# Performance work log

Measured on AMD Instinct MI355X. Metric: run time of the kernel, lower is better.

## Reference

```python
import jax, jax.numpy as jnp
import numpy as np

# Mamba2 hyperparameters
D_MODEL = 768
D_STATE = 64
D_CONV = 4
EXPAND = 2
HEADDIM = 64
CHUNK = 64
D_INNER = EXPAND * D_MODEL            # 1536
NHEADS = D_INNER // HEADDIM           # 24
D_IN_PROJ = 2 * D_INNER + 2 * D_STATE + NHEADS  # 3224
CONV_DIM = D_INNER + 2 * D_STATE      # 1664
B_SZ = 8
SEQ = 4096  # multiple of CHUNK -> no padding branch


def setup_inputs() -> dict:
    key = jax.random.key(0)
    ks = jax.random.split(key, 6)
    u = jax.random.normal(ks[0], (B_SZ, SEQ, D_MODEL), jnp.float32)
    # fan-in scaled weights (matches nn.Linear/Conv1d default init scale)
    W_in = jax.random.normal(ks[1], (D_IN_PROJ, D_MODEL), jnp.float32) / np.sqrt(D_MODEL).astype(np.float32)
    conv_w = jax.random.normal(ks[2], (CONV_DIM, 1, D_CONV), jnp.float32) / np.sqrt(D_CONV).astype(np.float32)
    conv_b = jnp.zeros((CONV_DIM,), jnp.float32)
    dt_bias = jax.random.uniform(ks[3], (NHEADS,), jnp.float32, -4.0, 1.0)  # nn.init.uniform_(-4, 1)
    A_log = jnp.full((NHEADS,), -np.log(2.0), jnp.float32)                  # nn.init.constant_(-log 2)
    D_param = jnp.ones((NHEADS,), jnp.float32)
    norm_w = jnp.ones((D_INNER,), jnp.float32)
    W_out = jax.random.normal(ks[4], (D_MODEL, D_INNER), jnp.float32) / np.sqrt(D_INNER).astype(np.float32)
    return dict(u=u, W_in=W_in, conv_w=conv_w, conv_b=conv_b, dt_bias=dt_bias,
                A_log=A_log, D_param=D_param, norm_w=norm_w, W_out=W_out)


def _segsum(x):
    """Stable segment sum: out[..., i, j] = sum_{j < k <= i} x[..., k]; -inf above diagonal."""
    T = x.shape[-1]
    lower_strict = jnp.tril(jnp.ones((T, T), bool), -1)
    xe = jnp.where(lower_strict, x[..., :, None], 0.0)   # broadcast x over last (col) axis
    s = jnp.cumsum(xe, axis=-2)
    lower = jnp.tril(jnp.ones((T, T), bool), 0)
    return jnp.where(lower, s, -jnp.inf)


def _ssd(x, A, B, C, chunk):
    """Chunked SSD. x:(b,L,h,p)  A:(b,L,h)  B,C:(b,L,1,n)."""
    b, L, h, p = x.shape
    c = L // chunk
    n = B.shape[-1]
    x = x.reshape(b, c, chunk, h, p)
    A = A.reshape(b, c, chunk, h).transpose(0, 3, 1, 2)   # b h c l
    B = B.reshape(b, c, chunk, 1, n)
    C = C.reshape(b, c, chunk, 1, n)
    A_cs = jnp.cumsum(A, axis=-1)                          # b h c l
    # intra-chunk (diagonal) term
    Lmat = jnp.exp(_segsum(A))                             # b h c l s
    Y_diag = jnp.einsum('bclhn,bcshn,bhcls,bcshp->bclhp', C, B, Lmat, x)
    # per-chunk states
    decay_states = jnp.exp(A_cs[..., -1:] - A_cs)          # b h c l
    states = jnp.einsum('bclhn,bhcl,bclhp->bchpn', B, decay_states, x)
    states = jnp.concatenate([jnp.zeros_like(states[:, :1]), states], axis=1)  # b (c+1) h p n
    # inter-chunk recurrence
    A_last = jnp.pad(A_cs[..., -1], ((0, 0), (0, 0), (1, 0)))  # b h (c+1)
    decay_chunk = jnp.exp(_segsum(A_last))                     # b h (c+1) (c+1)
    new_states = jnp.einsum('bhzc,bchpn->bzhpn', decay_chunk, states)
    states = new_states[:, :-1]                                # b c h p n
    # off-diagonal (state-to-output) term
    Y_off = jnp.einsum('bclhn,bchpn,bhcl->bclhp', C, states, jnp.exp(A_cs))
    return (Y_diag + Y_off).reshape(b, L, h, p)


def reference(u, W_in, conv_w, conv_b, dt_bias, A_log, D_param, norm_w, W_out):
    b, L, _ = u.shape  # L % CHUNK == 0, so pad branch is a no-op
    zxbcdt = u @ W_in.T                                    # (b, L, D_IN_PROJ)
    z = zxbcdt[..., :D_INNER]
    xBC = zxbcdt[..., D_INNER:D_INNER + CONV_DIM]
    dt = jax.nn.softplus(zxbcdt[..., D_INNER + CONV_DIM:] + dt_bias)  # (b, L, h)
    # causal depthwise conv1d (torch pads both sides by d_conv-1 then slices [:L] == left pad)
    xBC = jax.lax.conv_general_dilated(
        xBC.transpose(0, 2, 1), conv_w, window_strides=(1,),
        padding=[(D_CONV - 1, 0)], dimension_numbers=('NCH', 'OIH', 'NCH'),
        feature_group_count=CONV_DIM)
    xBC = jax.nn.silu(xBC.transpose(0, 2, 1) + conv_b)     # (b, L, CONV_DIM)
    x = xBC[..., :D_INNER].reshape(b, L, NHEADS, HEADDIM)
    Bm = xBC[..., D_INNER:D_INNER + D_STATE][:, :, None, :]  # (b, L, 1, n)
    Cm = xBC[..., D_INNER + D_STATE:][:, :, None, :]
    A = -jnp.exp(A_log)                                    # (h,)
    Y = _ssd(x * dt[..., None], A * dt, Bm, Cm, CHUNK)
    y = Y + x * D_param[:, None]                           # skip term
    y = y.reshape(b, L, D_INNER)
    # gated RMSNorm: x * silu(z), then rmsnorm * weight
    y = y * jax.nn.silu(z)
    y = y * jax.lax.rsqrt(jnp.mean(y * y, axis=-1, keepdims=True) + 1e-5) * norm_w
    return y @ W_out.T
```

## Files before the change

### kernel.cpp

```cpp
#include <hip/hip_runtime.h>
#include <stdint.h>

typedef unsigned short u16;
typedef __bf16 bf16x8 __attribute__((ext_vector_type(8)));
typedef float f32x4 __attribute__((ext_vector_type(4)));
typedef unsigned short u16x8 __attribute__((ext_vector_type(8)));
typedef unsigned short u16x4 __attribute__((ext_vector_type(4)));
typedef __attribute__((address_space(1))) unsigned int gu32;
typedef __attribute__((address_space(3))) unsigned int lu32;

__device__ __forceinline__ float bf2f(u16 u){ unsigned int v=((unsigned int)u)<<16; float f; __builtin_memcpy(&f,&v,4); return f; }
__device__ __forceinline__ u16 f2bf(float f){ unsigned int v; __builtin_memcpy(&v,&f,4); v += 0x7fffu + ((v>>16)&1u); return (u16)(v>>16); }
__device__ __forceinline__ int swz(int r,int c){ return (r<<6) + (c ^ ((r&7)<<3)); }
__device__ __forceinline__ void glds16(const void* g, void* l){
  __builtin_amdgcn_global_load_lds((gu32*)g, (lu32*)l, 16, 0, 0);
}

__global__ __launch_bounds__(256) void k_cast(const float* __restrict__ in, u16* __restrict__ out, int n4){
  int i = blockIdx.x*256 + threadIdx.x;
  if (i >= n4) return;
  const f32x4 v = *(const f32x4*)(in + (size_t)i*4);
  u16x4 o; o.x=f2bf(v.x); o.y=f2bf(v.y); o.z=f2bf(v.z); o.w=f2bf(v.w);
  *(u16x4*)(out + (size_t)i*4) = o;
}

__global__ __launch_bounds__(256) void k_cast_pad(const float* __restrict__ in, u16* __restrict__ out){
  int i = blockIdx.x*256 + threadIdx.x;
  int e0 = i*4;
  int row = e0 / 768;
  int col = e0 - row*768;
  u16x4 o;
  if (row < 3224){
    const f32x4 v = *(const f32x4*)(in + (size_t)row*768 + col);
    o.x=f2bf(v.x); o.y=f2bf(v.y); o.z=f2bf(v.z); o.w=f2bf(v.w);
  } else { o.x=0; o.y=0; o.z=0; o.w=0; }
  *(u16x4*)(out + e0) = o;
}

template<int K, int EPI>
__global__ __launch_bounds__(256,2) void k_gemm(
    const u16* __restrict__ A, const u16* __restrict__ Bw,
    u16* __restrict__ o_z, u16* __restrict__ o_xbc, float* __restrict__ o_dt,
    const float* __restrict__ dt_bias, float* __restrict__ o_f32)
{
  __shared__ __align__(16) u16 Alds[8192];
  __shared__ __align__(16) u16 Blds[8192];
  const int tid = threadIdx.x;
  const int wave = tid>>6, lane = tid&63;
  const int m0 = blockIdx.x<<7, n0 = blockIdx.y<<7;
  const int wr = (wave>>1)<<6, wc = (wave&1)<<6;
  const int srow = tid>>3, sc0 = (tid&7)<<3;
  const int lo16 = lane&15, hi = lane>>4;
  f32x4 acc[4][4] = {};
  for (int k0 = 0; k0 < K; k0 += 64){
    #pragma unroll
    for (int i = 0; i < 4; ++i){
      const int row = (i<<5) + srow;
      const int scol = sc0 ^ ((row&7)<<3);
      glds16(A  + (size_t)(m0+row)*K + k0 + scol, &Alds[(i<<11) + (wave<<9)]);
      glds16(Bw + (size_t)(n0+row)*K + k0 + scol, &Blds[(i<<11) + (wave<<9)]);
    }
    __syncthreads();
    #pragma unroll
    for (int kk = 0; kk < 2; ++kk){
      const int kb = (kk<<5) + (hi<<3);
      bf16x8 af[4], bfv[4];
      #pragma unroll
      for (int m = 0; m < 4; ++m){
        const int r = wr + (m<<4) + lo16;
        af[m] = *(const bf16x8*)&Alds[(r<<6) + (kb ^ ((r&7)<<3))];
      }
      #pragma unroll
      for (int n = 0; n < 4; ++n){
        const int r = wc + (n<<4) + lo16;
        bfv[n] = *(const bf16x8*)&Blds[(r<<6) + (kb ^ ((r&7)<<3))];
      }
      #pragma unroll
      for (int m = 0; m < 4; ++m)
      #pragma unroll
      for (int n = 0; n < 4; ++n)
        acc[m][n] = __builtin_amdgcn_mfma_f32_16x16x32_bf16(af[m], bfv[n], acc[m][n], 0,0,0);
    }
    __syncthreads();
  }
  #pragma unroll
  for (int m = 0; m < 4; ++m)
  #pragma unroll
  for (int n = 0; n < 4; ++n)
  #pragma unroll
  for (int i = 0; i < 4; ++i){
    const int gr = m0 + wr + (m<<4) + (hi<<2) + i;
    const int gc = n0 + wc + (n<<4) + lo16;
    const float v = acc[m][n][i];
    if constexpr (EPI == 0){
      if (gc < 1536)      o_z[(size_t)gr*1536 + gc] = f2bf(v);
      else if (gc < 3200) o_xbc[(size_t)gr*1664 + (gc-1536)] = f2bf(v);
      else if (gc < 3224){
        const float t = v + dt_bias[gc-3200];
        o_dt[(size_t)gr*24 + (gc-3200)] = (t > 20.f) ? t : log1pf(__expf(t));
      }
    } else {
      o_f32[(size_t)gr*768 + gc] = v;
    }
  }
}

__global__ __launch_bounds__(256) void k_conv(
    const u16* __restrict__ xbc, const float* __restrict__ cw, const float* __restrict__ cb,
    u16* __restrict__ xo, u16* __restrict__ Bo, u16* __restrict__ Co)
{
  const int idx = blockIdx.x*256 + threadIdx.x;
  if (idx >= 4096*208) return;
  const int g  = idx % 208;
  const int pt = idx / 208;
  const int ch0 = g << 3;
  const int m0 = pt << 3;
  const int l0 = m0 & 4095;
  float wgt[8][4], bias[8];
  #pragma unroll
  for (int j = 0; j < 8; ++j){
    const f32x4 wv = *(const f32x4*)(cw + (size_t)(ch0+j)*4);
    wgt[j][0]=wv.x; wgt[j][1]=wv.y; wgt[j][2]=wv.z; wgt[j][3]=wv.w;
    bias[j] = cb[ch0+j];
  }
  float acc[8][8];
  #pragma unroll
  for (int p = 0; p < 8; ++p)
  #pragma unroll
  for (int j = 0; j < 8; ++j) acc[p][j] = bias[j];
  #pragma unroll
  for (int r = -3; r < 8; ++r){
    const int ls = l0 + r;
    if (ls < 0) continue;
    const u16x8 v = *(const u16x8*)(xbc + (size_t)(m0+r)*1664 + ch0);
    float xf[8];
    #pragma unroll
    for (int j = 0; j < 8; ++j) xf[j] = bf2f(v[j]);
    #pragma unroll
    for (int t = 0; t < 4; ++t){
      const int p = r + 3 - t;
      if (p < 0 || p > 7) continue;
      #pragma unroll
      for (int j = 0; j < 8; ++j) acc[p][j] += xf[j] * wgt[j][t];
    }
  }
  #pragma unroll
  for (int p = 0; p < 8; ++p){
    u16x8 o;
    #pragma unroll
    for (int j = 0; j < 8; ++j){ const float s = acc[p][j]; o[j] = f2bf(s / (1.f + __expf(-s))); }
    const size_t m = m0 + p;
    if (ch0 < 1536)      *(u16x8*)(xo + m*1536 + ch0)      = o;
    else if (ch0 < 1600) *(u16x8*)(Bo + m*64 + (ch0-1536)) = o;
    else                 *(u16x8*)(Co + m*64 + (ch0-1600)) = o;
  }
}

__global__ __launch_bounds__(256,1) void k_ssd(
    const u16* __restrict__ xc, const u16* __restrict__ Bg, const u16* __restrict__ Cg,
    const float* __restrict__ dtg, const float* __restrict__ A_log,
    const float* __restrict__ Dp, u16* __restrict__ yo)
{
  __shared__ __align__(16) u16 Bn[4096], Bdt[4096], Cn[4096], Cd[4096], xdtT[4096], xls[4096], Ml[4096], Sbf[4096];
  __shared__ float Sst[4096];
  __shared__ float df[64], Acs[64];
  const int tid = threadIdx.x, wave = tid>>6, lane = tid&63;
  const int lo16 = lane&15, hi = lane>>4;
  const int b = blockIdx.x / 24, h = blockIdx.x % 24;
  const float Ah = -__expf(A_log[h]);
  const float Dh = Dp[h];
  for (int i = tid; i < 4096; i += 256){ Sst[i]=0.f; Sbf[i]=0; }
  const int lrow = tid>>2, c16 = (tid&3)<<4;
  const size_t bx  = (size_t)b*4096*1536 + (size_t)h*64;
  const size_t bbc = (size_t)b*4096*64;
  const size_t bdt = (size_t)b*4096*24 + h;

  for (int c = 0; c < 64; ++c){
    const int l0 = c<<6;
    if (tid < 64) df[tid] = dtg[bdt + (size_t)(l0+tid)*24];
    __syncthreads();
    if (wave == 0){
      float s = Ah * df[lane];
      #pragma unroll
      for (int off = 1; off < 64; off <<= 1){
        const float t = __shfl_up(s, off);
        if (lane >= off) s += t;
      }
      Acs[lane] = s;
    }
    __syncthreads();
    const float Alast = Acs[63];
    {
      const float dtl = df[lrow];
      const float dec = __expf(Alast - Acs[lrow]);
      const float el  = __expf(Acs[lrow]);
      const u16* gx  = xc + bx  + (size_t)(l0+lrow)*1536 + c16;
      const u16* gb  = Bg + bbc + (size_t)(l0+lrow)*64 + c16;
      const u16* gcp = Cg + bbc + (size_t)(l0+lrow)*64 + c16;
      const u16x8 x0 = *(const u16x8*)gx;      const u16x8 x1 = *(const u16x8*)(gx+8);
      const u16x8 b0 = *(const u16x8*)gb;      const u16x8 b1 = *(const u16x8*)(gb+8);
      const u16x8 c0 = *(const u16x8*)gcp;     const u16x8 c1 = *(const u16x8*)(gcp+8);
      #pragma unroll
      for (int j = 0; j < 8; ++j){
        const int p = c16 + j, q = c16 + 8 + j;
        xls[swz(lrow,p)]  = x0[j];                         xls[swz(lrow,q)]  = x1[j];
        xdtT[swz(p,lrow)] = f2bf(bf2f(x0[j]) * dtl);       xdtT[swz(q,lrow)] = f2bf(bf2f(x1[j]) * dtl);
        Bn[swz(lrow,p)]   = b0[j];                         Bn[swz(lrow,q)]   = b1[j];
        Bdt[swz(p,lrow)]  = f2bf(bf2f(b0[j]) * dec);       Bdt[swz(q,lrow)]  = f2bf(bf2f(b1[j]) * dec);
        Cn[swz(lrow,p)]   = c0[j];                         Cn[swz(lrow,q)]   = c1[j];
        Cd[swz(lrow,p)]   = f2bf(bf2f(c0[j]) * el);        Cd[swz(lrow,q)]   = f2bf(bf2f(c1[j]) * el);
      }
    }
    __syncthreads();
    f32x4 accG[4] = {};
    #pragma unroll
    for (int kk = 0; kk < 2; ++kk){
      const int kb = (kk<<5) + (hi<<3);
      const int rA = (wave<<4) + lo16;
      const bf16x8 a = *(const bf16x8*)&Cn[(rA<<6) + (kb ^ ((rA&7)<<3))];
      #pragma unroll
      for (int t = 0; t < 4; ++t){
        const int rb = (t<<4) + lo16;
        const bf16x8 bb = *(const bf16x8*)&Bn[(rb<<6) + (kb ^ ((rb&7)<<3))];
        accG[t] = __builtin_amdgcn_mfma_f32_16x16x32_bf16(a, bb, accG[t], 0,0,0);
      }
    }
    #pragma unroll
    for (int t = 0; t < 4; ++t)
    #pragma unroll
    for (int i = 0; i < 4; ++i){
      const int r = (wave<<4) + (hi<<2) + i;
      const int s = (t<<4) + lo16;
      const float v = (s <= r) ? accG[t][i] * __expf(Acs[r] - Acs[s]) : 0.f;
      Ml[swz(r,s)] = f2bf(v);
    }
    f32x4 accY[4] = {}, accS[4] = {};
    #pragma unroll
    for (int kk = 0; kk < 2; ++kk){
      const int kb = (kk<<5) + (hi<<3);
      const int rA = (wave<<4) + lo16;
      const int oA = (rA<<6) + (kb ^ ((rA&7)<<3));
      const bf16x8 aM = *(const bf16x8*)&Ml[oA];
      const bf16x8 aC = *(const bf16x8*)&Cd[oA];
      const bf16x8 aX = *(const bf16x8*)&xdtT[oA];
      #pragma unroll
      for (int t = 0; t < 4; ++t){
        const int rb = (t<<4) + lo16;
        const int o = (rb<<6) + (kb ^ ((rb&7)<<3));
        const bf16x8 bX = *(const bf16x8*)&xdtT[o];
        const bf16x8 bS = *(const bf16x8*)&Sbf[o];
        const bf16x8 bB = *(const bf16x8*)&Bdt[o];
        accY[t] = __builtin_amdgcn_mfma_f32_16x16x32_bf16(aM, bX, accY[t], 0,0,0);
        accY[t] = __builtin_amdgcn_mfma_f32_16x16x32_bf16(aC, bS, accY[t], 0,0,0);
        accS[t] = __builtin_amdgcn_mfma_f32_16x16x32_bf16(aX, bB, accS[t], 0,0,0);
      }
    }
    __syncthreads();
    const float lam = __expf(Alast);
    #pragma unroll
    for (int t = 0; t < 4; ++t)
    #pragma unroll
    for (int i = 0; i < 4; ++i){
      const int p = (wave<<4) + (hi<<2) + i;
      const int n = (t<<4) + lo16;
      const float s = Sst[(p<<6)+n] * lam + accS[t][i];
      Sst[(p<<6)+n] = s;
      Sbf[swz(p,n)] = f2bf(s);
    }
    #pragma unroll
    for (int t = 0; t < 4; ++t)
    #pragma unroll
    for (int i = 0; i < 4; ++i){
      const int r = (wave<<4) + (hi<<2) + i;
      const int p = (t<<4) + lo16;
      const float y = accY[t][i] + bf2f(xls[swz(r,p)]) * Dh;
      yo[bx + (size_t)(l0+r)*1536 + p] = f2bf(y);
    }
  }
}

__global__ __launch_bounds__(192) void k_gnorm(
    const u16* __restrict__ y, const u16* __restrict__ z,
    const float* __restrict__ nw, u16* __restrict__ out)
{
  __shared__ float red[3];
  const int m = blockIdx.x, t = threadIdx.x;
  const size_t base = (size_t)m*1536 + t*8;
  const u16x8 yv = *(const u16x8*)(y + base);
  const u16x8 zv = *(const u16x8*)(z + base);
  float vals[8]; float ss = 0.f;
  #pragma unroll
  for (int j = 0; j < 8; ++j){
    const float zf = bf2f(zv[j]);
    const float v = bf2f(yv[j]) * zf / (1.f + __expf(-zf));
    vals[j] = v; ss += v*v;
  }
  #pragma unroll
  for (int off = 32; off > 0; off >>= 1) ss += __shfl_down(ss, off);
  if ((t & 63) == 0) red[t>>6] = ss;
  __syncthreads();
  const float sc = rsqrtf((red[0]+red[1]+red[2]) * (1.f/1536.f) + 1e-5f);
  u16x8 o;
  #pragma unroll
  for (int j = 0; j < 8; ++j) o[j] = f2bf(vals[j] * sc * nw[t*8+j]);
  *(u16x8*)(out + base) = o;
}

extern "C" void kernel_launch(void* const* d_in, const int* in_sizes, int n_in,
                              void* d_out, int out_size, void* d_ws, size_t ws_size,
                              hipStream_t stream)
{
  const float* u       = (const float*)d_in[0];
  const float* W_in    = (const float*)d_in[1];
  const float* conv_w  = (const float*)d_in[2];
  const float* conv_b  = (const float*)d_in[3];
  const float* dt_bias = (const float*)d_in[4];
  const float* A_log   = (const float*)d_in[5];
  const float* D_param = (const float*)d_in[6];
  const float* norm_w  = (const float*)d_in[7];
  const float* W_out   = (const float*)d_in[8];
  (void)in_sizes; (void)n_in; (void)out_size;
  if (ws_size < (size_t)379715584) return;

  char* w = (char*)d_ws;
  size_t off = 0;
  auto alloc = [&](size_t bytes)->void*{ void* p = w + off; off += (bytes + 255) & ~(size_t)255; return p; };
  u16* ubf    = (u16*)alloc(50331648);
  u16* winbf  = (u16*)alloc(5111808);
  u16* woutbf = (u16*)alloc(2359296);
  u16* zbf    = (u16*)alloc(100663296);
  u16* xbcbf  = (u16*)alloc(109051904);
  float* dtbuf= (float*)alloc(3145728);
  u16* xconv  = (u16*)alloc(100663296);
  u16* Bbuf   = (u16*)alloc(4194304);
  u16* Cbuf   = (u16*)alloc(4194304);
  u16* yssd   = xbcbf;
  u16* ynorm  = xconv;

  k_cast<<<24576, 256, 0, stream>>>(u, ubf, 6291456);
  k_cast_pad<<<2496, 256, 0, stream>>>(W_in, winbf);
  k_cast<<<1152, 256, 0, stream>>>(W_out, woutbf, 294912);
  k_gemm<768,0><<<dim3(256,26), 256, 0, stream>>>(ubf, winbf, zbf, xbcbf, dtbuf, dt_bias, nullptr);
  k_conv<<<3328, 256, 0, stream>>>(xbcbf, conv_w, conv_b, xconv, Bbuf, Cbuf);
  k_ssd<<<192, 256, 0, stream>>>(xconv, Bbuf, Cbuf, dtbuf, A_log, D_param, yssd);
  k_gnorm<<<32768, 192, 0, stream>>>(yssd, zbf, norm_w, ynorm);
  k_gemm<1536,1><<<dim3(256,6), 256, 0, stream>>>(ynorm, woutbf, nullptr, nullptr, nullptr, nullptr, (float*)d_out);
}
```

Baseline: 752.4 us.

## Pre-swizzle SSD operands in conv and double-buffer chunk loads in SSD

The conv kernel now writes x*dt transposed and pre-swizzled per chunk, plus B in normal and transposed form and C in normal form, and dt is stored head-major. The SSD kernel then streams these tiles into LDS with async global_load_lds, double-buffered so the next chunk's loads overlap compute. It also folds the D skip term into the diagonal of the intra-chunk matrix (Dh/dt) and applies decay and exp scaling at use time. This removes the per-chunk scalar transpose-and-scale LDS stores and serial global load latency from the 192-block SSD kernel, at the cost of more conv output writes, manual waitcnt tuning, and a possible precision change from dividing by dt in bf16.

```diff
diff --git a/kernel.cpp b/kernel.cpp
--- a/kernel.cpp
+++ b/kernel.cpp
@@ -97,7 +97,7 @@
       else if (gc < 3200) o_xbc[(size_t)gr*1664 + (gc-1536)] = f2bf(v);
       else if (gc < 3224){
         const float t = v + dt_bias[gc-3200];
-        o_dt[(size_t)gr*24 + (gc-3200)] = (t > 20.f) ? t : log1pf(__expf(t));
+        o_dt[(size_t)(gc-3200)*32768 + gr] = (t > 20.f) ? t : log1pf(__expf(t));
       }
     } else {
       o_f32[(size_t)gr*768 + gc] = v;
@@ -107,7 +107,8 @@
 
 __global__ __launch_bounds__(256) void k_conv(
     const u16* __restrict__ xbc, const float* __restrict__ cw, const float* __restrict__ cb,
-    u16* __restrict__ xo, u16* __restrict__ Bo, u16* __restrict__ Co)
+    const float* __restrict__ dtT,
+    u16* __restrict__ xT, u16* __restrict__ Bn, u16* __restrict__ BT, u16* __restrict__ Cn)
 {
   const int idx = blockIdx.x*256 + threadIdx.x;
   if (idx >= 4096*208) return;
@@ -116,18 +117,18 @@
   const int ch0 = g << 3;
   const int m0 = pt << 3;
   const int l0 = m0 & 4095;
-  float wgt[8][4], bias[8];
+  float wgt[8][4], bias8[8];
   #pragma unroll
   for (int j = 0; j < 8; ++j){
     const f32x4 wv = *(const f32x4*)(cw + (size_t)(ch0+j)*4);
     wgt[j][0]=wv.x; wgt[j][1]=wv.y; wgt[j][2]=wv.z; wgt[j][3]=wv.w;
-    bias[j] = cb[ch0+j];
+    bias8[j] = cb[ch0+j];
   }
   float acc[8][8];
   #pragma unroll
   for (int p = 0; p < 8; ++p)
   #pragma unroll
-  for (int j = 0; j < 8; ++j) acc[p][j] = bias[j];
+  for (int j = 0; j < 8; ++j) acc[p][j] = bias8[j];
   #pragma unroll
   for (int r = -3; r < 8; ++r){
     const int ls = l0 + r;
@@ -145,83 +146,128 @@
     }
   }
   #pragma unroll
-  for (int p = 0; p < 8; ++p){
-    u16x8 o;
-    #pragma unroll
-    for (int j = 0; j < 8; ++j){ const float s = acc[p][j]; o[j] = f2bf(s / (1.f + __expf(-s))); }
-    const size_t m = m0 + p;
-    if (ch0 < 1536)      *(u16x8*)(xo + m*1536 + ch0)      = o;
-    else if (ch0 < 1600) *(u16x8*)(Bo + m*64 + (ch0-1536)) = o;
-    else                 *(u16x8*)(Co + m*64 + (ch0-1600)) = o;
+  for (int p = 0; p < 8; ++p)
+  #pragma unroll
+  for (int j = 0; j < 8; ++j){ const float s = acc[p][j]; acc[p][j] = s / (1.f + __expf(-s)); }
+
+  const int b = m0 >> 12;
+  const int cch = l0 >> 6;
+  const int lr0 = l0 & 63;
+  if (ch0 < 1536){
+    const int h = ch0 >> 6, p0 = ch0 & 63;
+    const f32x4 d0 = *(const f32x4*)(dtT + (size_t)h*32768 + m0);
+    const f32x4 d1 = *(const f32x4*)(dtT + (size_t)h*32768 + m0 + 4);
+    const float dtl[8] = {d0.x,d0.y,d0.z,d0.w,d1.x,d1.y,d1.z,d1.w};
+    const size_t rb = (size_t)(b*24+h)*64;
+    #pragma unroll
+    for (int j = 0; j < 8; ++j){
+      const int row = p0 + j;
+      u16x8 o;
+      #pragma unroll
+      for (int p = 0; p < 8; ++p) o[p] = f2bf(acc[p][j] * dtl[p]);
+      *(u16x8*)(xT + (rb + row)*4096 + (size_t)cch*64 + (lr0 ^ ((row&7)<<3))) = o;
+    }
+  } else if (ch0 < 1600){
+    const int n0 = ch0 - 1536;
+    const size_t tb = ((size_t)(b*64 + cch))*4096;
+    #pragma unroll
+    for (int p = 0; p < 8; ++p){
+      const int lr = lr0 + p;
+      u16x8 o;
+      #pragma unroll
+      for (int j = 0; j < 8; ++j) o[j] = f2bf(acc[p][j]);
+      *(u16x8*)(Bn + tb + lr*64 + (n0 ^ ((lr&7)<<3))) = o;
+    }
+    #pragma unroll
+    for (int j = 0; j < 8; ++j){
+      const int row = n0 + j;
+      u16x8 o;
+      #pragma unroll
+      for (int p = 0; p < 8; ++p) o[p] = f2bf(acc[p][j]);
+      *(u16x8*)(BT + tb + row*64 + (lr0 ^ ((row&7)<<3))) = o;
+    }
+  } else {
+    const int n0 = ch0 - 1600;
+    const size_t tb = ((size_t)(b*64 + cch))*4096;
+    #pragma unroll
+    for (int p = 0; p < 8; ++p){
+      const int lr = lr0 + p;
+      u16x8 o;
+      #pragma unroll
+      for (int j = 0; j < 8; ++j) o[j] = f2bf(acc[p][j]);
+      *(u16x8*)(Cn + tb + lr*64 + (n0 ^ ((lr&7)<<3))) = o;
+    }
   }
 }
 
 __global__ __launch_bounds__(256,1) void k_ssd(
-    const u16* __restrict__ xc, const u16* __restrict__ Bg, const u16* __restrict__ Cg,
-    const float* __restrict__ dtg, const float* __restrict__ A_log,
+    const u16* __restrict__ xT, const u16* __restrict__ Bn, const u16* __restrict__ BT,
+    const u16* __restrict__ Cn, const float* __restrict__ dtT, const float* __restrict__ A_log,
     const float* __restrict__ Dp, u16* __restrict__ yo)
 {
-  __shared__ __align__(16) u16 Bn[4096], Bdt[4096], Cn[4096], Cd[4096], xdtT[4096], xls[4096], Ml[4096], Sbf[4096];
+  __shared__ __align__(16) u16 tiles[2][4][4096];
+  __shared__ __align__(16) u16 Ml[4096];
+  __shared__ __align__(16) u16 Sbf[4096];
   __shared__ float Sst[4096];
-  __shared__ float df[64], Acs[64];
+  __shared__ float df[64], Acs[64], decs[64], els[64];
   const int tid = threadIdx.x, wave = tid>>6, lane = tid&63;
   const int lo16 = lane&15, hi = lane>>4;
   const int b = blockIdx.x / 24, h = blockIdx.x % 24;
   const float Ah = -__expf(A_log[h]);
   const float Dh = Dp[h];
   for (int i = tid; i < 4096; i += 256){ Sst[i]=0.f; Sbf[i]=0; }
-  const int lrow = tid>>2, c16 = (tid&3)<<4;
-  const size_t bx  = (size_t)b*4096*1536 + (size_t)h*64;
-  const size_t bbc = (size_t)b*4096*64;
-  const size_t bdt = (size_t)b*4096*24 + h;
+  const size_t xTg  = (size_t)(b*24+h)*64*4096;
+  const size_t bcg  = (size_t)b*64*4096;
+  const size_t dtg0 = (size_t)h*32768 + (size_t)b*4096;
+  const size_t yb   = (size_t)b*4096*1536 + (size_t)h*64;
+
+  auto stage = [&](int buf, int c){
+    u16* dst = &tiles[buf][wave][0];
+    if (wave == 0){
+      const u16* g0 = xT + xTg + (size_t)c*64 + (size_t)(lane>>3)*4096 + (lane&7)*8;
+      #pragma unroll
+      for (int s = 0; s < 8; ++s) glds16(g0 + (size_t)s*32768, dst + s*512);
+    } else {
+      const u16* src = (wave==1 ? Bn : wave==2 ? BT : Cn) + bcg + (size_t)c*4096 + lane*8;
+      #pragma unroll
+      for (int s = 0; s < 8; ++s) glds16(src + s*512, dst + s*512);
+    }
+  };
+
+  float dtc = dtT[dtg0 + lane];
+  stage(0, 0);
 
   for (int c = 0; c < 64; ++c){
-    const int l0 = c<<6;
-    if (tid < 64) df[tid] = dtg[bdt + (size_t)(l0+tid)*24];
-    __syncthreads();
-    if (wave == 0){
-      float s = Ah * df[lane];
-      #pragma unroll
-      for (int off = 1; off < 64; off <<= 1){
-        const float t = __shfl_up(s, off);
-        if (lane >= off) s += t;
-      }
-      Acs[lane] = s;
-    }
-    __syncthreads();
-    const float Alast = Acs[63];
-    {
-      const float dtl = df[lrow];
-      const float dec = __expf(Alast - Acs[lrow]);
-      const float el  = __expf(Acs[lrow]);
-      const u16* gx  = xc + bx  + (size_t)(l0+lrow)*1536 + c16;
-      const u16* gb  = Bg + bbc + (size_t)(l0+lrow)*64 + c16;
-      const u16* gcp = Cg + bbc + (size_t)(l0+lrow)*64 + c16;
-      const u16x8 x0 = *(const u16x8*)gx;      const u16x8 x1 = *(const u16x8*)(gx+8);
-      const u16x8 b0 = *(const u16x8*)gb;      const u16x8 b1 = *(const u16x8*)(gb+8);
-      const u16x8 c0 = *(const u16x8*)gcp;     const u16x8 c1 = *(const u16x8*)(gcp+8);
-      #pragma unroll
-      for (int j = 0; j < 8; ++j){
-        const int p = c16 + j, q = c16 + 8 + j;
-        xls[swz(lrow,p)]  = x0[j];                         xls[swz(lrow,q)]  = x1[j];
-        xdtT[swz(p,lrow)] = f2bf(bf2f(x0[j]) * dtl);       xdtT[swz(q,lrow)] = f2bf(bf2f(x1[j]) * dtl);
-        Bn[swz(lrow,p)]   = b0[j];                         Bn[swz(lrow,q)]   = b1[j];
-        Bdt[swz(p,lrow)]  = f2bf(bf2f(b0[j]) * dec);       Bdt[swz(q,lrow)]  = f2bf(bf2f(b1[j]) * dec);
-        Cn[swz(lrow,p)]   = c0[j];                         Cn[swz(lrow,q)]   = c1[j];
-        Cd[swz(lrow,p)]   = f2bf(bf2f(c0[j]) * el);        Cd[swz(lrow,q)]   = f2bf(bf2f(c1[j]) * el);
-      }
-    }
-    __syncthreads();
+    float s = Ah * dtc;
+    #pragma unroll
+    for (int o = 1; o < 64; o <<= 1){ const float t = __shfl_up(s, o); if (lane >= o) s += t; }
+    const float Alast = __shfl(s, 63);
+    const float lam = __expf(Alast);
+    if (wave == 0){ df[lane] = dtc; Acs[lane] = s; decs[lane] = __expf(Alast - s); els[lane] = __expf(s); }
+    if (c < 63){
+      dtc = dtT[dtg0 + (size_t)(c+1)*64 + lane];
+      stage((c+1)&1, c+1);
+    }
+    if (c == 0)       asm volatile("s_waitcnt vmcnt(0) lgkmcnt(0)" ::: "memory");
+    else if (c == 63) asm volatile("s_waitcnt vmcnt(16) lgkmcnt(0)" ::: "memory");
+    else              asm volatile("s_waitcnt vmcnt(25) lgkmcnt(0)" ::: "memory");
+    __builtin_amdgcn_s_barrier();
+
+    const u16* tx = &tiles[c&1][0][0];
+    const u16* tb = &tiles[c&1][1][0];
+    const u16* tt = &tiles[c&1][2][0];
+    const u16* tc = &tiles[c&1][3][0];
+
     f32x4 accG[4] = {};
     #pragma unroll
     for (int kk = 0; kk < 2; ++kk){
       const int kb = (kk<<5) + (hi<<3);
       const int rA = (wave<<4) + lo16;
-      const bf16x8 a = *(const bf16x8*)&Cn[(rA<<6) + (kb ^ ((rA&7)<<3))];
+      const bf16x8 a = *(const bf16x8*)&tc[(rA<<6) + (kb ^ ((rA&7)<<3))];
       #pragma unroll
       for (int t = 0; t < 4; ++t){
         const int rb = (t<<4) + lo16;
-        const bf16x8 bb = *(const bf16x8*)&Bn[(rb<<6) + (kb ^ ((rb&7)<<3))];
+        const bf16x8 bb = *(const bf16x8*)&tb[(rb<<6) + (kb ^ ((rb&7)<<3))];
         accG[t] = __builtin_amdgcn_mfma_f32_16x16x32_bf16(a, bb, accG[t], 0,0,0);
       }
     }
@@ -230,42 +276,51 @@
     #pragma unroll
     for (int i = 0; i < 4; ++i){
       const int r = (wave<<4) + (hi<<2) + i;
-      const int s = (t<<4) + lo16;
-      const float v = (s <= r) ? accG[t][i] * __expf(Acs[r] - Acs[s]) : 0.f;
-      Ml[swz(r,s)] = f2bf(v);
-    }
-    f32x4 accY[4] = {}, accS[4] = {};
+      const int sc = (t<<4) + lo16;
+      float v = 0.f;
+      if (sc <= r) v = accG[t][i] * __expf(Acs[r] - Acs[sc]);
+      if (sc == r) v += Dh / df[r];
+      Ml[swz(r,sc)] = f2bf(v);
+    }
+    f32x4 aYd[4] = {}, aYo[4] = {}, aS[4] = {};
     #pragma unroll
     for (int kk = 0; kk < 2; ++kk){
       const int kb = (kk<<5) + (hi<<3);
       const int rA = (wave<<4) + lo16;
       const int oA = (rA<<6) + (kb ^ ((rA&7)<<3));
       const bf16x8 aM = *(const bf16x8*)&Ml[oA];
-      const bf16x8 aC = *(const bf16x8*)&Cd[oA];
-      const bf16x8 aX = *(const bf16x8*)&xdtT[oA];
+      const bf16x8 aC = *(const bf16x8*)&tc[oA];
+      const u16x8  aXu = *(const u16x8*)&tx[oA];
+      u16x8 aXsu;
+      #pragma unroll
+      for (int j = 0; j < 8; ++j) aXsu[j] = f2bf(bf2f(aXu[j]) * decs[kb + j]);
+      const bf16x8 aXs = *(const bf16x8*)&aXsu;
       #pragma unroll
       for (int t = 0; t < 4; ++t){
         const int rb = (t<<4) + lo16;
         const int o = (rb<<6) + (kb ^ ((rb&7)<<3));
-        const bf16x8 bX = *(const bf16x8*)&xdtT[o];
+        const bf16x8 bX = *(const bf16x8*)&tx[o];
         const bf16x8 bS = *(const bf16x8*)&Sbf[o];
-        const bf16x8 bB = *(const bf16x8*)&Bdt[o];
-        accY[t] = __builtin_amdgcn_mfma_f32_16x16x32_bf16(aM, bX, accY[t], 0,0,0);
-        accY[t] = __builtin_amdgcn_mfma_f32_16x16x32_bf16(aC, bS, accY[t], 0,0,0);
-        accS[t] = __builtin_amdgcn_mfma_f32_16x16x32_bf16(aX, bB, accS[t], 0,0,0);
+        const bf16x8 bB = *(const bf16x8*)&tt[o];
+        aYd[t] = __builtin_amdgcn_mfma_f32_16x16x32_bf16(aM, bX, aYd[t], 0,0,0);
+        aYo[t] = __builtin_amdgcn_mfma_f32_16x16x32_bf16(aC, bS, aYo[t], 0,0,0);
+        aS[t]  = __builtin_amdgcn_mfma_f32_16x16x32_bf16(aXs, bB, aS[t], 0,0,0);
       }
     }
-    __syncthreads();
-    const float lam = __expf(Alast);
+    float el4[4];
+    #pragma unroll
+    for (int i = 0; i < 4; ++i) el4[i] = els[(wave<<4) + (hi<<2) + i];
+    asm volatile("s_waitcnt lgkmcnt(0)" ::: "memory");
+    __builtin_amdgcn_s_barrier();
     #pragma unroll
     for (int t = 0; t < 4; ++t)
     #pragma unroll
     for (int i = 0; i < 4; ++i){
       const int p = (wave<<4) + (hi<<2) + i;
       const int n = (t<<4) + lo16;
-      const float s = Sst[(p<<6)+n] * lam + accS[t][i];
-      Sst[(p<<6)+n] = s;
-      Sbf[swz(p,n)] = f2bf(s);
+      const float sv = Sst[(p<<6)+n] * lam + aS[t][i];
+      Sst[(p<<6)+n] = sv;
+      Sbf[swz(p,n)] = f2bf(sv);
     }
     #pragma unroll
     for (int t = 0; t < 4; ++t)
@@ -273,8 +328,8 @@
     for (int i = 0; i < 4; ++i){
       const int r = (wave<<4) + (hi<<2) + i;
       const int p = (t<<4) + lo16;
-      const float y = accY[t][i] + bf2f(xls[swz(r,p)]) * Dh;
-      yo[bx + (size_t)(l0+r)*1536 + p] = f2bf(y);
+      const float y = aYd[t][i] + el4[i] * aYo[t][i];
+      yo[yb + (size_t)((c<<6)+r)*1536 + p] = f2bf(y);
     }
   }
 }
@@ -330,19 +385,20 @@
   u16* woutbf = (u16*)alloc(2359296);
   u16* zbf    = (u16*)alloc(100663296);
   u16* xbcbf  = (u16*)alloc(109051904);
-  float* dtbuf= (float*)alloc(3145728);
-  u16* xconv  = (u16*)alloc(100663296);
-  u16* Bbuf   = (u16*)alloc(4194304);
-  u16* Cbuf   = (u16*)alloc(4194304);
+  float* dtT  = (float*)alloc(3145728);
+  u16* xTb    = (u16*)alloc(100663296);
+  u16* Bnb    = (u16*)alloc(4194304);
+  u16* Cnb    = (u16*)alloc(4194304);
+  u16* BTb    = ubf;
   u16* yssd   = xbcbf;
-  u16* ynorm  = xconv;
+  u16* ynorm  = xTb;
 
   k_cast<<<24576, 256, 0, stream>>>(u, ubf, 6291456);
   k_cast_pad<<<2496, 256, 0, stream>>>(W_in, winbf);
   k_cast<<<1152, 256, 0, stream>>>(W_out, woutbf, 294912);
-  k_gemm<768,0><<<dim3(256,26), 256, 0, stream>>>(ubf, winbf, zbf, xbcbf, dtbuf, dt_bias, nullptr);
-  k_conv<<<3328, 256, 0, stream>>>(xbcbf, conv_w, conv_b, xconv, Bbuf, Cbuf);
-  k_ssd<<<192, 256, 0, stream>>>(xconv, Bbuf, Cbuf, dtbuf, A_log, D_param, yssd);
+  k_gemm<768,0><<<dim3(256,26), 256, 0, stream>>>(ubf, winbf, zbf, xbcbf, dtT, dt_bias, nullptr);
+  k_conv<<<3328, 256, 0, stream>>>(xbcbf, conv_w, conv_b, dtT, xTb, Bnb, BTb, Cnb);
+  k_ssd<<<192, 256, 0, stream>>>(xTb, Bnb, BTb, Cnb, dtT, A_log, D_param, yssd);
   k_gnorm<<<32768, 192, 0, stream>>>(yssd, zbf, norm_w, ynorm);
   k_gemm<1536,1><<<dim3(256,6), 256, 0, stream>>>(ynorm, woutbf, nullptr, nullptr, nullptr, nullptr, (float*)d_out);
 }
```

New measurement: 773.4 us. 2.8% more time.
